# Kernel tuning notes

Hardware: AMD Instinct MI355X
Metric: run time of the kernel (lower is better)

The kernel has to match this reference:

```python
import jax, jax.numpy as jnp
import numpy as np

B, S, H = 64, 2048, 768
LAM = 0.0  # sparsegen-lin lambda (lam=0 -> sparsemax)
NEG = -1e30


def setup_inputs() -> dict:
    key = jax.random.key(0)
    k1, k2, k3, k4, k5 = jax.random.split(key, 5)
    hidden = jax.random.normal(k1, (B, S, H), jnp.float32)
    # contiguous entity spans of random length (>=16 valid tokens per example)
    lengths = jax.random.randint(k2, (B,), 16, S)
    mask1d = (jnp.arange(S)[None, :] < lengths[:, None]).astype(jnp.float32)
    token_mask = jnp.broadcast_to(mask1d[:, :, None], (B, S, H))
    pooled_tokens = jax.random.normal(k3, (B, H), jnp.float32)
    w_align = jax.random.normal(k4, (2 * H,), jnp.float32) * 0.02
    b_align = jax.random.normal(k5, (1,), jnp.float32) * 0.02
    return {"hidden": hidden, "token_mask": token_mask,
            "pooled_tokens": pooled_tokens, "w_align": w_align, "b_align": b_align}


def sparsegen_masked(scores, valid, lam):
    """Batched sparsegen-lin over valid positions only.
    scores: [B, S] float, valid: [B, S] bool. Returns probs [B, S] (0 at invalid).
    Matches per-example torch SparsegenLin applied to masked_select'd scores.
    """
    n = scores.shape[-1]
    zmax = jnp.max(jnp.where(valid, scores, -jnp.inf), axis=-1, keepdims=True)
    z = scores - zmax                                # subtract max over valid
    z_sortable = jnp.where(valid, z, NEG)
    zs = -jnp.sort(-z_sortable, axis=-1)             # descending; valid first
    n_valid = jnp.sum(valid, axis=-1, keepdims=True)
    ks = jnp.arange(1, n + 1, dtype=scores.dtype)[None, :]
    sorted_valid = ks <= n_valid.astype(scores.dtype)
    zs_m = jnp.where(sorted_valid, zs, 0.0)
    csum = jnp.cumsum(zs_m, axis=-1)
    bound = 1.0 - lam + ks * zs_m
    is_gt = (bound > csum) & sorted_valid
    k = jnp.maximum(jnp.max(jnp.where(is_gt, ks, 0.0), axis=-1, keepdims=True), 1.0)
    tau = (jnp.sum(jnp.where(is_gt, zs_m, 0.0), axis=-1, keepdims=True) - 1.0 + lam) / k
    ps = jnp.maximum((z - tau) / (1.0 - lam), 0.0)
    return jnp.where(valid, ps, 0.0)


def reference(hidden, token_mask, pooled_tokens, w_align, b_align):
    masked_hidden = hidden * token_mask                       # [B,S,H]
    tokens_rep_masked = pooled_tokens[:, None, :] * token_mask  # [B,S,H]
    # alignment_model(cat(tokens_rep_masked, masked_hidden)) -> [B,S]
    scores = (jnp.einsum('bsh,h->bs', tokens_rep_masked, w_align[:H])
              + jnp.einsum('bsh,h->bs', masked_hidden, w_align[H:])
              + b_align[0])
    attn_mask = token_mask[:, :, 0] > 0                       # [B,S] bool
    attention_probs = sparsegen_masked(scores, attn_mask, LAM)[:, :, None]  # [B,S,1]
    pooled = jnp.sum(masked_hidden * attention_probs, axis=1)  # [B,H]
    # insize == outsize -> output_layer is skipped (projected = pooled)
    return pooled, attention_probs
```

## Files before the change

### kernel.cpp

```cpp
#include <hip/hip_runtime.h>
#include <hip/hip_bf16.h>
#include <cstdint>
#include <cstddef>

#define BB 64
#define SS 2048
#define HH 768
#define LAM 0.0f
#define NEGV -1e30f

__global__ void scores_kernel(const float* __restrict__ hidden,
                              const float* __restrict__ token_mask,
                              const float* __restrict__ w_align,
                              float* __restrict__ scores) {
    int row = blockIdx.x * 4 + (threadIdx.x >> 6);
    int lane = threadIdx.x & 63;
    float m = token_mask[(size_t)row * HH];
    if (m == 0.0f) {
        if (lane == 0) scores[row] = NEGV;
        return;
    }
    const float* hrow = hidden + (size_t)row * HH;
    const float* w2 = w_align + HH;
    float acc = 0.f;
#pragma unroll
    for (int r = 0; r < 3; ++r) {
        int idx = r * 256 + lane * 4;
        float4 h = *reinterpret_cast<const float4*>(hrow + idx);
        float4 w = *reinterpret_cast<const float4*>(w2 + idx);
        acc += h.x * w.x + h.y * w.y + h.z * w.z + h.w * w.w;
    }
#pragma unroll
    for (int off = 32; off >= 1; off >>= 1) acc += __shfl_xor(acc, off);
    if (lane == 0) scores[row] = acc;
}

__global__ __launch_bounds__(256, 1) void tau_pool_kernel(
        const float* __restrict__ hidden,
        const float* __restrict__ pooled_tokens,
        const float* __restrict__ w_align,
        const float* __restrict__ b_align,
        const float* __restrict__ scores,
        float* __restrict__ out) {
    const int b = (blockIdx.x * 256 + threadIdx.x) >> 6;
    const int lane = threadIdx.x & 63;

    const float* pt = pooled_tokens + b * HH;
    float dp = 0.f;
#pragma unroll
    for (int i = 0; i < 3; ++i) {
        int idx = i * 256 + lane * 4;
        float4 a = *reinterpret_cast<const float4*>(pt + idx);
        float4 w = *reinterpret_cast<const float4*>(w_align + idx);
        dp += a.x * w.x + a.y * w.y + a.z * w.z + a.w * w.w;
    }
#pragma unroll
    for (int off = 32; off >= 1; off >>= 1) dp += __shfl_xor(dp, off);
    dp += b_align[0];

    const float* sc = scores + b * SS;
    float z[32];
#pragma unroll
    for (int i = 0; i < 8; ++i) {
        float4 v = *reinterpret_cast<const float4*>(sc + i * 256 + lane * 4);
        z[i * 4 + 0] = v.x + dp;
        z[i * 4 + 1] = v.y + dp;
        z[i * 4 + 2] = v.z + dp;
        z[i * 4 + 3] = v.w + dp;
    }

    float mx = z[0];
#pragma unroll
    for (int i = 1; i < 32; ++i) mx = fmaxf(mx, z[i]);
#pragma unroll
    for (int off = 32; off >= 1; off >>= 1) mx = fmaxf(mx, __shfl_xor(mx, off));
#pragma unroll
    for (int i = 0; i < 32; ++i) z[i] -= mx;

    float tau = -1.0f;
#pragma unroll 1
    for (int it = 0; it < 50; ++it) {
        float a = 0.f, c = 0.f;
#pragma unroll
        for (int i = 0; i < 32; ++i) {
            bool g = z[i] > tau;
            a += g ? z[i] : 0.f;
            c += g ? 1.f : 0.f;
        }
#pragma unroll
        for (int off = 32; off >= 1; off >>= 1) {
            a += __shfl_xor(a, off);
            c += __shfl_xor(c, off);
        }
        float tn = (a - 1.f + LAM) / c;
        if (tn == tau) break;
        tau = tn;
    }

    const float inv = 1.f / (1.f - LAM);
    float p[32];
#pragma unroll
    for (int i = 0; i < 32; ++i) p[i] = fmaxf((z[i] - tau) * inv, 0.f);
    float* po = out + BB * HH + b * SS;
#pragma unroll
    for (int i = 0; i < 8; ++i) {
        float4 v = make_float4(p[i * 4 + 0], p[i * 4 + 1], p[i * 4 + 2], p[i * 4 + 3]);
        *reinterpret_cast<float4*>(po + i * 256 + lane * 4) = v;
    }

    float acc[12];
#pragma unroll
    for (int j = 0; j < 12; ++j) acc[j] = 0.f;
    const float* hb = hidden + (size_t)b * SS * HH;
#pragma unroll 1
    for (int i = 0; i < 8; ++i) {
#pragma unroll 1
        for (int c = 0; c < 4; ++c) {
            float pv = p[i * 4 + c];
            unsigned long long m = __ballot(pv > 0.f);
            while (m) {
                int src = __ffsll((long long)m) - 1;
                m &= m - 1;
                float pb = __shfl(pv, src);
                int sidx = i * 256 + src * 4 + c;
                const float* hrow = hb + (size_t)sidx * HH;
#pragma unroll
                for (int j = 0; j < 12; ++j)
                    acc[j] += pb * hrow[j * 64 + lane];
            }
        }
    }
#pragma unroll
    for (int j = 0; j < 12; ++j)
        out[b * HH + j * 64 + lane] = acc[j];
}

extern "C" void kernel_launch(void* const* d_in, const int* in_sizes, int n_in,
                              void* d_out, int out_size, void* d_ws, size_t ws_size,
                              hipStream_t stream) {
    const float* hidden        = (const float*)d_in[0];
    const float* token_mask    = (const float*)d_in[1];
    const float* pooled_tokens = (const float*)d_in[2];
    const float* w_align       = (const float*)d_in[3];
    const float* b_align       = (const float*)d_in[4];
    float* out = (float*)d_out;

    float* scores_ws;
    if (ws_size >= (size_t)BB * SS * sizeof(float)) {
        scores_ws = (float*)d_ws;
    } else {
        scores_ws = out + BB * HH;
    }

    scores_kernel<<<dim3((BB * SS) / 4), dim3(256), 0, stream>>>(
        hidden, token_mask, w_align, scores_ws);

    tau_pool_kernel<<<dim3(16), dim3(256), 0, stream>>>(
        hidden, pooled_tokens, w_align, b_align, scores_ws, out);
}
```

Measured before the change: 49.37 us.

## Compact nonzero sparsemax weights to LDS and pool with one block per batch

The tau/pool kernel now runs one 768-thread block per batch row instead of one wavefront per row across 16 blocks. Wave 0 computes tau and compacts the nonzero probabilities and their indices into shared memory. Then all threads each own one hidden column and accumulate four rows per iteration. This spreads the gather over many more CUs and threads and exposes more memory-level parallelism. The cost is a block barrier and more LDS use, while the other 11 waves sit idle during the tau computation.

```diff
diff --git a/kernel.cpp b/kernel.cpp
--- a/kernel.cpp
+++ b/kernel.cpp
@@ -35,104 +35,125 @@
     if (lane == 0) scores[row] = acc;
 }
 
-__global__ __launch_bounds__(256, 1) void tau_pool_kernel(
+__global__ __launch_bounds__(768, 1) void tau_pool_kernel(
         const float* __restrict__ hidden,
         const float* __restrict__ pooled_tokens,
         const float* __restrict__ w_align,
         const float* __restrict__ b_align,
         const float* __restrict__ scores,
         float* __restrict__ out) {
-    const int b = (blockIdx.x * 256 + threadIdx.x) >> 6;
-    const int lane = threadIdx.x & 63;
+    __shared__ int   s_idx[SS];
+    __shared__ float s_p[SS];
+    __shared__ int   s_cnt;
 
-    const float* pt = pooled_tokens + b * HH;
-    float dp = 0.f;
+    const int b = blockIdx.x;
+    const int t = threadIdx.x;
+    const int lane = t & 63;
+    const int wv = t >> 6;
+
+    if (wv == 0) {
+        const float* pt = pooled_tokens + b * HH;
+        float dp = 0.f;
 #pragma unroll
-    for (int i = 0; i < 3; ++i) {
-        int idx = i * 256 + lane * 4;
-        float4 a = *reinterpret_cast<const float4*>(pt + idx);
-        float4 w = *reinterpret_cast<const float4*>(w_align + idx);
-        dp += a.x * w.x + a.y * w.y + a.z * w.z + a.w * w.w;
-    }
-#pragma unroll
-    for (int off = 32; off >= 1; off >>= 1) dp += __shfl_xor(dp, off);
-    dp += b_align[0];
-
-    const float* sc = scores + b * SS;
-    float z[32];
-#pragma unroll
-    for (int i = 0; i < 8; ++i) {
-        float4 v = *reinterpret_cast<const float4*>(sc + i * 256 + lane * 4);
-        z[i * 4 + 0] = v.x + dp;
-        z[i * 4 + 1] = v.y + dp;
-        z[i * 4 + 2] = v.z + dp;
-        z[i * 4 + 3] = v.w + dp;
-    }
-
-    float mx = z[0];
-#pragma unroll
-    for (int i = 1; i < 32; ++i) mx = fmaxf(mx, z[i]);
-#pragma unroll
-    for (int off = 32; off >= 1; off >>= 1) mx = fmaxf(mx, __shfl_xor(mx, off));
-#pragma unroll
-    for (int i = 0; i < 32; ++i) z[i] -= mx;
-
-    float tau = -1.0f;
-#pragma unroll 1
-    for (int it = 0; it < 50; ++it) {
-        float a = 0.f, c = 0.f;
-#pragma unroll
-        for (int i = 0; i < 32; ++i) {
-            bool g = z[i] > tau;
-            a += g ? z[i] : 0.f;
-            c += g ? 1.f : 0.f;
+        for (int i = 0; i < 3; ++i) {
+            int idx = i * 256 + lane * 4;
+            float4 a = *reinterpret_cast<const float4*>(pt + idx);
+            float4 w = *reinterpret_cast<const float4*>(w_align + idx);
+            dp += a.x * w.x + a.y * w.y + a.z * w.z + a.w * w.w;
         }
 #pragma unroll
-        for (int off = 32; off >= 1; off >>= 1) {
-            a += __shfl_xor(a, off);
-            c += __shfl_xor(c, off);
+        for (int off = 32; off >= 1; off >>= 1) dp += __shfl_xor(dp, off);
+        dp += b_align[0];
+
+        const float* sc = scores + b * SS;
+        float z[32];
+#pragma unroll
+        for (int i = 0; i < 8; ++i) {
+            float4 v = *reinterpret_cast<const float4*>(sc + i * 256 + lane * 4);
+            z[i * 4 + 0] = v.x + dp;
+            z[i * 4 + 1] = v.y + dp;
+            z[i * 4 + 2] = v.z + dp;
+            z[i * 4 + 3] = v.w + dp;
         }
-        float tn = (a - 1.f + LAM) / c;
-        if (tn == tau) break;
-        tau = tn;
-    }
 
-    const float inv = 1.f / (1.f - LAM);
-    float p[32];
+        float mx = z[0];
 #pragma unroll
-    for (int i = 0; i < 32; ++i) p[i] = fmaxf((z[i] - tau) * inv, 0.f);
-    float* po = out + BB * HH + b * SS;
+        for (int i = 1; i < 32; ++i) mx = fmaxf(mx, z[i]);
 #pragma unroll
-    for (int i = 0; i < 8; ++i) {
-        float4 v = make_float4(p[i * 4 + 0], p[i * 4 + 1], p[i * 4 + 2], p[i * 4 + 3]);
-        *reinterpret_cast<float4*>(po + i * 256 + lane * 4) = v;
-    }
+        for (int off = 32; off >= 1; off >>= 1) mx = fmaxf(mx, __shfl_xor(mx, off));
+#pragma unroll
+        for (int i = 0; i < 32; ++i) z[i] -= mx;
 
-    float acc[12];
+        float tau = -1.0f;
+#pragma unroll 1
+        for (int it = 0; it < 50; ++it) {
+            float a = 0.f, c = 0.f;
 #pragma unroll
-    for (int j = 0; j < 12; ++j) acc[j] = 0.f;
-    const float* hb = hidden + (size_t)b * SS * HH;
-#pragma unroll 1
-    for (int i = 0; i < 8; ++i) {
-#pragma unroll 1
-        for (int c = 0; c < 4; ++c) {
-            float pv = p[i * 4 + c];
-            unsigned long long m = __ballot(pv > 0.f);
-            while (m) {
-                int src = __ffsll((long long)m) - 1;
-                m &= m - 1;
-                float pb = __shfl(pv, src);
-                int sidx = i * 256 + src * 4 + c;
-                const float* hrow = hb + (size_t)sidx * HH;
+            for (int i = 0; i < 32; ++i) {
+                bool g = z[i] > tau;
+                a += g ? z[i] : 0.f;
+                c += g ? 1.f : 0.f;
+            }
 #pragma unroll
-                for (int j = 0; j < 12; ++j)
-                    acc[j] += pb * hrow[j * 64 + lane];
+            for (int off = 32; off >= 1; off >>= 1) {
+                a += __shfl_xor(a, off);
+                c += __shfl_xor(c, off);
+            }
+            float tn = (a - 1.f + LAM) / c;
+            if (tn == tau) break;
+            tau = tn;
+        }
+
+        const float inv = 1.f / (1.f - LAM);
+        float p[32];
+#pragma unroll
+        for (int i = 0; i < 32; ++i) p[i] = fmaxf((z[i] - tau) * inv, 0.f);
+        float* po = out + BB * HH + b * SS;
+#pragma unroll
+        for (int i = 0; i < 8; ++i) {
+            float4 v = make_float4(p[i * 4 + 0], p[i * 4 + 1], p[i * 4 + 2], p[i * 4 + 3]);
+            *reinterpret_cast<float4*>(po + i * 256 + lane * 4) = v;
+        }
+
+        int cnt = 0;
+#pragma unroll
+        for (int i = 0; i < 8; ++i) {
+#pragma unroll
+            for (int c = 0; c < 4; ++c) {
+                float pv = p[i * 4 + c];
+                unsigned long long m = __ballot(pv > 0.f);
+                if (pv > 0.f) {
+                    int pos = cnt + (int)__popcll(m & ((1ull << lane) - 1ull));
+                    s_idx[pos] = i * 256 + lane * 4 + c;
+                    s_p[pos] = pv;
+                }
+                cnt += (int)__popcll(m);
             }
         }
+        if (lane == 0) s_cnt = cnt;
     }
-#pragma unroll
-    for (int j = 0; j < 12; ++j)
-        out[b * HH + j * 64 + lane] = acc[j];
+    __syncthreads();
+
+    const int cnt = s_cnt;
+    const float* hb = hidden + (size_t)b * SS * HH;
+    float acc = 0.f;
+#pragma unroll 1
+    for (int j = 0; j < cnt; j += 4) {
+        int   i0 = s_idx[j];
+        float p0 = s_p[j];
+        int   i1 = (j + 1 < cnt) ? s_idx[j + 1] : 0;
+        float p1 = (j + 1 < cnt) ? s_p[j + 1] : 0.f;
+        int   i2 = (j + 2 < cnt) ? s_idx[j + 2] : 0;
+        float p2 = (j + 2 < cnt) ? s_p[j + 2] : 0.f;
+        int   i3 = (j + 3 < cnt) ? s_idx[j + 3] : 0;
+        float p3 = (j + 3 < cnt) ? s_p[j + 3] : 0.f;
+        float h0 = hb[(size_t)i0 * HH + t];
+        float h1 = hb[(size_t)i1 * HH + t];
+        float h2 = hb[(size_t)i2 * HH + t];
+        float h3 = hb[(size_t)i3 * HH + t];
+        acc += p0 * h0 + p1 * h1 + p2 * h2 + p3 * h3;
+    }
+    out[b * HH + t] = acc;
 }
 
 extern "C" void kernel_launch(void* const* d_in, const int* in_sizes, int n_in,
@@ -155,6 +176,6 @@
     scores_kernel<<<dim3((BB * SS) / 4), dim3(256), 0, stream>>>(
         hidden, token_mask, w_align, scores_ws);
 
-    tau_pool_kernel<<<dim3(16), dim3(256), 0, stream>>>(
+    tau_pool_kernel<<<dim3(BB), dim3(768), 0, stream>>>(
         hidden, pooled_tokens, w_align, b_align, scores_ws, out);
 }
```

Result: faster. 47.18 us (-4.4%).
